# Optimization experiments

Hardware: AMD Instinct MI355X
Metric: run time of the kernel (lower is better)

Reference implementation:

```python
import jax, jax.numpy as jnp
import numpy as np

B, D, H = 256, 512, 256
K = 5
MARGIN = 1.0
TAU = 1.0
LAM_C = 0.01
LAM_E = 0.1
BETA = 0.1
LN_EPS = 1e-5


def _layernorm(x, g, b):
    mu = jnp.mean(x, axis=-1, keepdims=True)
    var = jnp.var(x, axis=-1, keepdims=True)
    return (x - mu) * jax.lax.rsqrt(var + LN_EPS) * g + b


def setup_inputs() -> dict:
    key = jax.random.key(0)
    ks = jax.random.split(key, 16)
    s = 0.02
    inp = {
        "outputs": jax.random.normal(ks[0], (B, 3, 64, 64), jnp.float32),
        "images": jax.random.normal(ks[1], (B, 3, 64, 64), jnp.float32),
        "f_orig": jax.random.normal(ks[2], (B, D), jnp.float32),
        "f_recon": jax.random.normal(ks[3], (B, D), jnp.float32),
        "cf1": jax.random.normal(ks[4], (B, 256, 8, 8), jnp.float32),
        "cf2": jax.random.normal(ks[5], (B, 512, 4, 4), jnp.float32),
        # EnergyNet encoder params
        "W1": jax.random.normal(ks[6], (D, H), jnp.float32) * s,
        "b1": jnp.zeros((H,), jnp.float32),
        "g1": jnp.ones((H,), jnp.float32),
        "be1": jnp.zeros((H,), jnp.float32),
        "W2": jax.random.normal(ks[7], (H, H), jnp.float32) * s,
        "b2": jnp.zeros((H,), jnp.float32),
        # EnergyNet interaction params
        "W3": jax.random.normal(ks[8], (3 * H, H), jnp.float32) * s,
        "b3": jnp.zeros((H,), jnp.float32),
        "g3": jnp.ones((H,), jnp.float32),
        "be3": jnp.zeros((H,), jnp.float32),
        "W4": jax.random.normal(ks[9], (H, H // 2), jnp.float32) * s,
        "b4": jnp.zeros((H // 2,), jnp.float32),
        "W5": jax.random.normal(ks[10], (H // 2, 1), jnp.float32) * s,
        "b5": jnp.zeros((1,), jnp.float32),
    }
    return inp


def _encoder(x, W1, b1, g1, be1, W2, b2):
    h = _layernorm(x @ W1 + b1, g1, be1)
    return jax.nn.relu(h) @ W2 + b2


def _energy_matrix(f1, f2, W1, b1, g1, be1, W2, b2, W3, b3, g3, be3, W4, b4, W5, b5):
    e1 = _encoder(f1, W1, b1, g1, be1, W2, b2)  # [B,H]
    e2 = _encoder(f2, W1, b1, g1, be1, W2, b2)  # [B,H]
    e1b = jnp.broadcast_to(e1[:, None, :], (B, B, H))
    e2b = jnp.broadcast_to(e2[None, :, :], (B, B, H))
    combined = jnp.concatenate([e1b, e2b, e1b * e2b], axis=-1)  # [B,B,3H]
    h = jax.nn.relu(_layernorm(combined @ W3 + b3, g3, be3))
    h = jax.nn.relu(h @ W4 + b4)
    return (h @ W5 + b5)[..., 0]  # [B,B]


def _topk_neighbors(f, k):
    fn = f / (jnp.linalg.norm(f, axis=1, keepdims=True))
    sim = fn @ fn.T
    sim = jnp.where(jnp.eye(f.shape[0], dtype=bool), -jnp.inf, sim)
    _, idx = jax.lax.top_k(sim, k)  # [B,k]
    onehot = jnp.zeros((f.shape[0], f.shape[0]), jnp.float32)
    rows = jnp.arange(f.shape[0])[:, None]
    return onehot.at[rows, idx].set(1.0)


def _entropy(x):
    xn = (x - x.min()) / (x.max() - x.min() + 1e-8)
    # torch.histc(bins=256, min=0, max=1): values at max go to last bin
    idx = jnp.clip(jnp.floor(xn.reshape(-1) * 256.0).astype(jnp.int32), 0, 255)
    hist = jnp.bincount(idx, length=256).astype(jnp.float32)
    p = hist / hist.sum()
    return -jnp.sum(p * jnp.log2(p + 1e-8))


def reference(outputs, images, f_orig, f_recon, cf1, cf2,
              W1, b1, g1, be1, W2, b2, W3, b3, g3, be3, W4, b4, W5, b5):
    # reconstruction loss
    recon = jnp.mean((outputs - images) ** 2)

    # energy margin loss
    E = _energy_matrix(f_orig, f_recon, W1, b1, g1, be1, W2, b2,
                       W3, b3, g3, be3, W4, b4, W5, b5)
    pos = jnp.diag(E)[:, None]
    losses = jax.nn.relu(MARGIN + E - pos)
    neg_mask = ~jnp.eye(B, dtype=bool)
    standard_loss = jnp.sum(losses * neg_mask) / (B * (B - 1))

    k = min(K, B - 1)
    on = _topk_neighbors(f_orig, k)
    rn = _topk_neighbors(f_recon, k)
    inter = jnp.sum(on * rn, axis=1)
    union = jnp.sum(jnp.clip(on + rn, 0.0, 1.0), axis=1)
    jaccard = inter / (union + 1e-8)
    neighbor_loss = 1.0 - jnp.mean(jaccard)
    energy_loss = standard_loss + 0.3 * neighbor_loss

    # compression loss over the dict of compressed features {cf1, cf2}
    sp = 0.5 * (jnp.mean(jnp.abs(cf1)) + jnp.mean(jnp.abs(cf2)))
    en = 0.5 * (_entropy(cf1) + _entropy(cf2))
    compress = sp + BETA * en

    total = recon + LAM_C * compress + LAM_E * energy_loss
    return (total, recon, energy_loss, compress)
```

## Files before the change

### kernel.cpp

```cpp
#include <hip/hip_runtime.h>
#include <math.h>

typedef __attribute__((ext_vector_type(8))) short short8;
typedef __attribute__((ext_vector_type(4))) float f32x4;
typedef __attribute__((ext_vector_type(4))) unsigned int u32x4;

union U8 { unsigned int u[4]; short8 s; u32x4 v; };


__device__ __forceinline__ float wave_sum(float v) {
#pragma unroll
    for (int o = 32; o > 0; o >>= 1) v += __shfl_down(v, o);
    return v;
}

__device__ __forceinline__ float block_sum256(float v, float* red) {
    v = wave_sum(v);
    int t = threadIdx.x;
    if ((t & 63) == 0) red[t >> 6] = v;
    __syncthreads();
    float r = red[0] + red[1] + red[2] + red[3];
    __syncthreads();
    return r;
}

__device__ __forceinline__ unsigned fenc(float f) {
    unsigned u = __float_as_uint(f);
    return (u & 0x80000000u) ? ~u : (u | 0x80000000u);
}
__device__ __forceinline__ float fdec(unsigned u) {
    return (u & 0x80000000u) ? __uint_as_float(u & 0x7fffffffu) : __uint_as_float(~u);
}

__device__ __forceinline__ ushort f2bf(float f) {
    unsigned u = __float_as_uint(f);
    unsigned r = (u + 0x7fffu + ((u >> 16) & 1u)) >> 16;
    return (ushort)r;
}
__device__ __forceinline__ float bflo(unsigned u) { return __uint_as_float(u << 16); }
__device__ __forceinline__ float bfhi(unsigned u) { return __uint_as_float(u & 0xffff0000u); }
__device__ __forceinline__ float bf2f(ushort u) { return __uint_as_float((unsigned)u << 16); }


__global__ void init_kernel(float* wsf, unsigned* wsu, int* wsi) {
    int t = threadIdx.x;
    if (t < 7) wsf[t] = 0.f;
    if (t == 7 || t == 9) wsu[t] = 0xFFFFFFFFu;
    if (t == 8 || t == 10) wsu[t] = 0u;
    wsi[16 + t] = 0;
    wsi[272 + t] = 0;
}

__device__ __forceinline__ void pack256(const float* __restrict__ src, ushort* __restrict__ dst, int s) {
    int lane = s & 63;
    int tt = (s >> 6) & 15;
    int kk = s >> 10;
    int qq = lane >> 4, nn = lane & 15;
    int tcol = tt * 16 + nn;
    short8 v;
#pragma unroll
    for (int jj = 0; jj < 8; ++jj) {
        int k = kk * 32 + qq * 8 + jj;
        v[jj] = (short)f2bf(src[(size_t)k * 256 + tcol]);
    }
    *(short8*)(dst + (size_t)s * 8) = v;
}

__device__ __forceinline__ void pack128(const float* __restrict__ src, ushort* __restrict__ dst, int s) {
    int lane = s & 63;
    int tt = (s >> 6) & 7;
    int kk = s >> 9;
    int qq = lane >> 4, nn = lane & 15;
    int ncol = tt * 16 + nn;
    short8 v;
#pragma unroll
    for (int jj = 0; jj < 8; ++jj) {
        int k = kk * 32 + qq * 8 + jj;
        v[jj] = (short)f2bf(src[(size_t)k * 128 + ncol]);
    }
    *(short8*)(dst + (size_t)s * 8) = v;
}

__global__ __launch_bounds__(256) void mega_kernel(
    const float4* __restrict__ o, const float4* __restrict__ im,
    const float4* __restrict__ cf1, const float4* __restrict__ cf2,
    const float* __restrict__ fo, const float* __restrict__ fr,
    const float* __restrict__ W1, const float* __restrict__ W2,
    const float* __restrict__ W3, const float* __restrict__ W4,
    float* wsf, unsigned* wsu, float* rnorm, float* fT,
    ushort* __restrict__ W3cpk, ushort* __restrict__ W4pk,
    ushort* __restrict__ W1pk, ushort* __restrict__ W2pk,
    ushort* __restrict__ W3apk, ushort* __restrict__ W3bpk) {
    __shared__ float smem[64 * 33];
    float* red = smem;
    int b = blockIdx.x, t = threadIdx.x;
    if (b < 208) {
        int pb = b;
        if (pb < 32) pack256(W3 + 512 * 256, W3cpk, pb * 256 + t);
        else if (pb < 48) pack128(W4, W4pk, (pb - 32) * 256 + t);
        else if (pb < 112) pack256(W1, W1pk, (pb - 48) * 256 + t);
        else if (pb < 144) pack256(W2, W2pk, (pb - 112) * 256 + t);
        else if (pb < 176) pack256(W3, W3apk, (pb - 144) * 256 + t);
        else pack256(W3 + 256 * 256, W3bpk, (pb - 176) * 256 + t);
    } else if (b < 336) {
        int bb = b - 208;
        int pass = bb >> 6;
        int kt = (bb >> 2) & 15;
        int jt = bb & 3;
        int k0 = kt * 32, j0 = jt * 64;
        const float* f = pass ? fr : fo;
        float (*tile)[33] = (float(*)[33])smem;
        int cl = t & 31, rl = t >> 5;
#pragma unroll
        for (int r = 0; r < 8; ++r) {
            int row = j0 + rl + r * 8;
            tile[rl + r * 8][cl] = f[(size_t)row * 512 + k0 + cl];
        }
        __syncthreads();
        int jl = t & 63, kq = t >> 6;
        float* dst = fT + (size_t)pass * 131072;
#pragma unroll
        for (int c = 0; c < 8; ++c) {
            int kl = kq * 8 + c;
            dst[(size_t)(k0 + kl) * 256 + j0 + jl] = tile[jl][kl];
        }
    } else {
        int bs = b - 336;
        if (bs < 512) {
            int base = bs * 1536 + t;
            float4 av[6], cv[6];
#pragma unroll
            for (int u = 0; u < 6; ++u) { av[u] = o[base + u * 256]; cv[u] = im[base + u * 256]; }
            float s0 = 0.f, s1 = 0.f;
#pragma unroll
            for (int u = 0; u < 6; ++u) {
                float dx = av[u].x - cv[u].x, dy = av[u].y - cv[u].y;
                float dz = av[u].z - cv[u].z, dw = av[u].w - cv[u].w;
                if (u & 1) s1 += dx * dx + dy * dy + dz * dz + dw * dw;
                else s0 += dx * dx + dy * dy + dz * dz + dw * dw;
            }
            float tot = block_sum256(s0 + s1, red);
            if (t == 0) atomicAdd(wsf + 0, tot);
        } else if (bs < 1536) {
            int which = (bs < 1024) ? 0 : 1;
            const float4* x = which ? cf2 : cf1;
            int niter = which ? 4 : 8;
            int base = which ? ((bs - 1024) * 1024 + t) : ((bs - 512) * 2048 + t);
            float4 v[8];
            for (int u = 0; u < niter; ++u) v[u] = x[base + u * 256];
            float s = 0.f, mn = INFINITY, mx = -INFINITY;
            for (int u = 0; u < niter; ++u) {
                float4 a = v[u];
                s += fabsf(a.x) + fabsf(a.y) + fabsf(a.z) + fabsf(a.w);
                mn = fminf(mn, fminf(fminf(a.x, a.y), fminf(a.z, a.w)));
                mx = fmaxf(mx, fmaxf(fmaxf(a.x, a.y), fmaxf(a.z, a.w)));
            }
            float tot = block_sum256(s, red);
#pragma unroll
            for (int off = 32; off > 0; off >>= 1) {
                mn = fminf(mn, __shfl_down(mn, off));
                mx = fmaxf(mx, __shfl_down(mx, off));
            }
            float* rmn = smem + 8;
            float* rmx = smem + 16;
            if ((t & 63) == 0) { rmn[t >> 6] = mn; rmx[t >> 6] = mx; }
            __syncthreads();
            if (t == 0) {
                atomicAdd(wsf + 1 + which, tot);
                float m1 = fminf(fminf(rmn[0], rmn[1]), fminf(rmn[2], rmn[3]));
                float m2 = fmaxf(fmaxf(rmx[0], rmx[1]), fmaxf(rmx[2], rmx[3]));
                atomicMin(wsu + 7 + which * 2, fenc(m1));
                atomicMax(wsu + 8 + which * 2, fenc(m2));
            }
        } else {
            int r = bs - 1536;
            const float4* f = (r < 256) ? ((const float4*)fo + (size_t)r * 128)
                                        : ((const float4*)fr + (size_t)(r - 256) * 128);
            float s = 0.f;
            if (t < 128) {
                float4 a = f[t];
                s = a.x * a.x + a.y * a.y + a.z * a.z + a.w * a.w;
            }
            float tot = block_sum256(s, red);
            if (t == 0) rnorm[r] = 1.0f / sqrtf(tot);
        }
    }
}

__global__ __launch_bounds__(256) void hist_kernel(const float4* __restrict__ cf1,
                                                   const float4* __restrict__ cf2,
                                                   const unsigned* wsu, int* wsi) {
    __shared__ int hl[256];
    int b = blockIdx.x, t = threadIdx.x;
    hl[t] = 0;
    __syncthreads();
    int which = (b < 512) ? 0 : 1;
    const float4* x = which ? cf2 : cf1;
    int niter = which ? 4 : 8;
    int base = which ? ((b - 512) * 1024 + t) : (b * 2048 + t);
    int* hist = wsi + (which ? 272 : 16);
    float mn = fdec(wsu[7 + which * 2]), mx = fdec(wsu[8 + which * 2]);
    float inv = 256.f / (mx - mn + 1e-8f);
    float4 v[8];
    for (int u = 0; u < niter; ++u) v[u] = x[base + u * 256];
    for (int u = 0; u < niter; ++u) {
        float4 a = v[u];
        int b0i = min(max((int)floorf((a.x - mn) * inv), 0), 255);
        int b1i = min(max((int)floorf((a.y - mn) * inv), 0), 255);
        int b2i = min(max((int)floorf((a.z - mn) * inv), 0), 255);
        int b3i = min(max((int)floorf((a.w - mn) * inv), 0), 255);
        atomicAdd(&hl[b0i], 1);
        atomicAdd(&hl[b1i], 1);
        atomicAdd(&hl[b2i], 1);
        atomicAdd(&hl[b3i], 1);
    }
    __syncthreads();
    if (hl[t]) atomicAdd(&hist[t], hl[t]);
}

__global__ __launch_bounds__(64, 1) void encoder_mfma(
    const float* __restrict__ fo, const float* __restrict__ fr,
    const ushort* __restrict__ W1p, const ushort* __restrict__ W2p,
    const ushort* __restrict__ W3ap, const ushort* __restrict__ W3bp,
    const float* __restrict__ b1, const float* __restrict__ g1,
    const float* __restrict__ be1, const float* __restrict__ b2,
    ushort* __restrict__ ebf, ushort* __restrict__ A1bf, ushort* __restrict__ A2bf)
{
    int lane = threadIdx.x & 63;
    int q = lane >> 4, n = lane & 15;
    int r = blockIdx.x * 16 + n;
    bool isOrig = (r < 256);
    const float* f = isOrig ? (fo + (size_t)r * 512) : (fr + (size_t)(r - 256) * 512);

    f32x4 acc[16];
#pragma unroll
    for (int tt = 0; tt < 16; ++tt) acc[tt] = (f32x4){0.f, 0.f, 0.f, 0.f};
    short8 wA[16], wB[16];
    {
        const ushort* wp0 = W1p + (size_t)lane * 8;
#pragma unroll
        for (int tt = 0; tt < 16; ++tt) wA[tt] = *(const short8*)(wp0 + (size_t)tt * 512);
    }
#pragma unroll
    for (int kk = 0; kk < 16; ++kk) {
        const short8* cur = (kk & 1) ? wB : wA;
        short8* nxt = (kk & 1) ? wA : wB;
        if (kk < 15) {
            const ushort* wpn = W1p + ((size_t)((kk + 1) * 1024 + lane)) * 8;
#pragma unroll
            for (int tt = 0; tt < 16; ++tt) nxt[tt] = *(const short8*)(wpn + (size_t)tt * 512);
        }
        int kb = kk * 32 + q * 8;
        float4 fa = *(const float4*)(f + kb);
        float4 fb = *(const float4*)(f + kb + 4);
        U8 bb;
        bb.u[0] = (unsigned)f2bf(fa.x) | ((unsigned)f2bf(fa.y) << 16);
        bb.u[1] = (unsigned)f2bf(fa.z) | ((unsigned)f2bf(fa.w) << 16);
        bb.u[2] = (unsigned)f2bf(fb.x) | ((unsigned)f2bf(fb.y) << 16);
        bb.u[3] = (unsigned)f2bf(fb.z) | ((unsigned)f2bf(fb.w) << 16);
#pragma unroll
        for (int tt = 0; tt < 16; ++tt)
            acc[tt] = __builtin_amdgcn_mfma_f32_16x16x32_bf16(cur[tt], bb.s, acc[tt], 0, 0, 0);
    }
    float s1 = 0.f, s2 = 0.f;
#pragma unroll
    for (int tt = 0; tt < 16; ++tt) {
        int tb = tt * 16 + q * 4;
        float4 bv = *(const float4*)(b1 + tb);
        float v0 = acc[tt][0] + bv.x, v1 = acc[tt][1] + bv.y;
        float v2 = acc[tt][2] + bv.z, v3 = acc[tt][3] + bv.w;
        acc[tt][0] = v0; acc[tt][1] = v1; acc[tt][2] = v2; acc[tt][3] = v3;
        s1 += v0 + v1 + v2 + v3;
        s2 += v0 * v0 + v1 * v1 + v2 * v2 + v3 * v3;
    }
    s1 += __shfl_xor(s1, 16); s1 += __shfl_xor(s1, 32);
    s2 += __shfl_xor(s2, 16); s2 += __shfl_xor(s2, 32);
    float mean = s1 * (1.f / 256.f);
    float var = s2 * (1.f / 256.f) - mean * mean;
    float rstd = rsqrtf(var + 1e-5f);
    uint2 pk[16];
#pragma unroll
    for (int tt = 0; tt < 16; ++tt) {
        int tb = tt * 16 + q * 4;
        float4 gg = *(const float4*)(g1 + tb);
        float4 be = *(const float4*)(be1 + tb);
        float h0 = fmaxf((acc[tt][0] - mean) * rstd * gg.x + be.x, 0.f);
        float h1 = fmaxf((acc[tt][1] - mean) * rstd * gg.y + be.y, 0.f);
        float h2 = fmaxf((acc[tt][2] - mean) * rstd * gg.z + be.z, 0.f);
        float h3 = fmaxf((acc[tt][3] - mean) * rstd * gg.w + be.w, 0.f);
        pk[tt].x = (unsigned)f2bf(h0) | ((unsigned)f2bf(h1) << 16);
        pk[tt].y = (unsigned)f2bf(h2) | ((unsigned)f2bf(h3) << 16);
    }

    int qh = (q >> 1) & 1;
    int src0 = ((q & 1) * 2) * 16 + n;
    int src1 = src0 + 16;

    f32x4 eacc[16];
#pragma unroll
    for (int tt = 0; tt < 16; ++tt) eacc[tt] = (f32x4){0.f, 0.f, 0.f, 0.f};
    {
        const ushort* wp0 = W2p + (size_t)lane * 8;
#pragma unroll
        for (int tt = 0; tt < 16; ++tt) wA[tt] = *(const short8*)(wp0 + (size_t)tt * 512);
    }
#pragma unroll
    for (int kk = 0; kk < 8; ++kk) {
        const short8* cur = (kk & 1) ? wB : wA;
        short8* nxt = (kk & 1) ? wA : wB;
        if (kk < 7) {
            const ushort* wpn = W2p + ((size_t)((kk + 1) * 1024 + lane)) * 8;
#pragma unroll
            for (int tt = 0; tt < 16; ++tt) nxt[tt] = *(const short8*)(wpn + (size_t)tt * 512);
        }
        uint2 lo2 = pk[kk * 2], hi2 = pk[kk * 2 + 1];
        unsigned a0 = (unsigned)__shfl((int)lo2.x, src0);
        unsigned a1 = (unsigned)__shfl((int)lo2.y, src0);
        unsigned b0 = (unsigned)__shfl((int)hi2.x, src0);
        unsigned b1v = (unsigned)__shfl((int)hi2.y, src0);
        unsigned c0 = (unsigned)__shfl((int)lo2.x, src1);
        unsigned c1 = (unsigned)__shfl((int)lo2.y, src1);
        unsigned d0 = (unsigned)__shfl((int)hi2.x, src1);
        unsigned d1 = (unsigned)__shfl((int)hi2.y, src1);
        U8 hb;
        hb.u[0] = qh ? b0 : a0;
        hb.u[1] = qh ? b1v : a1;
        hb.u[2] = qh ? d0 : c0;
        hb.u[3] = qh ? d1 : c1;
#pragma unroll
        for (int tt = 0; tt < 16; ++tt)
            eacc[tt] = __builtin_amdgcn_mfma_f32_16x16x32_bf16(cur[tt], hb.s, eacc[tt], 0, 0, 0);
    }
    uint2 epk[16];
#pragma unroll
    for (int tt = 0; tt < 16; ++tt) {
        int tb = tt * 16 + q * 4;
        float4 bv = *(const float4*)(b2 + tb);
        float e0 = eacc[tt][0] + bv.x, e1 = eacc[tt][1] + bv.y;
        float e2 = eacc[tt][2] + bv.z, e3 = eacc[tt][3] + bv.w;
        epk[tt].x = (unsigned)f2bf(e0) | ((unsigned)f2bf(e1) << 16);
        epk[tt].y = (unsigned)f2bf(e2) | ((unsigned)f2bf(e3) << 16);
        *(uint2*)(ebf + (size_t)r * 256 + tb) = epk[tt];
    }

    const ushort* W3x = isOrig ? W3ap : W3bp;
    f32x4 aacc[16];
#pragma unroll
    for (int tt = 0; tt < 16; ++tt) aacc[tt] = (f32x4){0.f, 0.f, 0.f, 0.f};
    {
        const ushort* wp0 = W3x + (size_t)lane * 8;
#pragma unroll
        for (int tt = 0; tt < 16; ++tt) wA[tt] = *(const short8*)(wp0 + (size_t)tt * 512);
    }
#pragma unroll
    for (int kk = 0; kk < 8; ++kk) {
        const short8* cur = (kk & 1) ? wB : wA;
        short8* nxt = (kk & 1) ? wA : wB;
        if (kk < 7) {
            const ushort* wpn = W3x + ((size_t)((kk + 1) * 1024 + lane)) * 8;
#pragma unroll
            for (int tt = 0; tt < 16; ++tt) nxt[tt] = *(const short8*)(wpn + (size_t)tt * 512);
        }
        uint2 lo2 = epk[kk * 2], hi2 = epk[kk * 2 + 1];
        unsigned a0 = (unsigned)__shfl((int)lo2.x, src0);
        unsigned a1 = (unsigned)__shfl((int)lo2.y, src0);
        unsigned b0 = (unsigned)__shfl((int)hi2.x, src0);
        unsigned b1v = (unsigned)__shfl((int)hi2.y, src0);
        unsigned c0 = (unsigned)__shfl((int)lo2.x, src1);
        unsigned c1 = (unsigned)__shfl((int)lo2.y, src1);
        unsigned d0 = (unsigned)__shfl((int)hi2.x, src1);
        unsigned d1 = (unsigned)__shfl((int)hi2.y, src1);
        U8 hb;
        hb.u[0] = qh ? b0 : a0;
        hb.u[1] = qh ? b1v : a1;
        hb.u[2] = qh ? d0 : c0;
        hb.u[3] = qh ? d1 : c1;
#pragma unroll
        for (int tt = 0; tt < 16; ++tt)
            aacc[tt] = __builtin_amdgcn_mfma_f32_16x16x32_bf16(cur[tt], hb.s, aacc[tt], 0, 0, 0);
    }
    ushort* dst = isOrig ? (A1bf + (size_t)r * 256) : (A2bf + (size_t)(r - 256) * 256);
#pragma unroll
    for (int tt = 0; tt < 16; ++tt) {
        int tb = tt * 16 + q * 4;
        uint2 pv;
        pv.x = (unsigned)f2bf(aacc[tt][0]) | ((unsigned)f2bf(aacc[tt][1]) << 16);
        pv.y = (unsigned)f2bf(aacc[tt][2]) | ((unsigned)f2bf(aacc[tt][3]) << 16);
        *(uint2*)(dst + tb) = pv;
    }
}

__global__ __launch_bounds__(256) void simtop_kernel(const float* __restrict__ fo,
                                                     const float* __restrict__ fr,
                                                     const float* __restrict__ rnorm,
                                                     const float* __restrict__ fT,
                                                     int* __restrict__ top5) {
    int b = blockIdx.x;
    int pass = b >> 7, pair = b & 127;
    int i0 = pair * 2, i1 = i0 + 1;
    const float* f = pass ? fr : fo;
    const float* rn = rnorm + pass * 256;
    __shared__ float2 fs2[512];
    __shared__ float candV[4][2][5];
    __shared__ int candI[4][2][5];
    int t = threadIdx.x;
    const float* f0 = f + (size_t)i0 * 512;
    const float* f1 = f + (size_t)i1 * 512;
    fs2[t] = make_float2(f0[t], f1[t]);
    fs2[t + 256] = make_float2(f0[t + 256], f1[t + 256]);
    __syncthreads();
    int j = t;
    const float* col = fT + (size_t)pass * 131072 + j;
    float x0 = 0.f, x1 = 0.f, y0 = 0.f, y1 = 0.f, z0 = 0.f, z1 = 0.f, u0 = 0.f, u1 = 0.f;
#pragma unroll 8
    for (int k = 0; k < 128; ++k) {
        float v0 = col[(size_t)k * 256];
        float v1 = col[(size_t)(k + 128) * 256];
        float v2 = col[(size_t)(k + 256) * 256];
        float v3 = col[(size_t)(k + 384) * 256];
        float2 g0 = fs2[k], g1 = fs2[k + 128], g2 = fs2[k + 256], g3 = fs2[k + 384];
        x0 += g0.x * v0; x1 += g0.y * v0;
        y0 += g1.x * v1; y1 += g1.y * v1;
        z0 += g2.x * v2; z1 += g2.y * v2;
        u0 += g3.x * v3; u1 += g3.y * v3;
    }
    float a0 = ((x0 + y0) + (z0 + u0)) * rn[j];
    float a1 = ((x1 + y1) + (z1 + u1)) * rn[j];
    if (j == i0) a0 = -INFINITY;
    if (j == i1) a1 = -INFINITY;
    int w = t >> 6, lane = t & 63;
    for (int sel = 0; sel < 2; ++sel) {
        float v2 = sel ? a1 : a0;
        int idx = j;
        for (int r = 0; r < 5; ++r) {
            float m = v2;
            int mi = idx;
#pragma unroll
            for (int off = 32; off > 0; off >>= 1) {
                float om = __shfl_xor(m, off);
                int omi = __shfl_xor(mi, off);
                if (om > m || (om == m && omi < mi)) { m = om; mi = omi; }
            }
            if (lane == 0) { candV[w][sel][r] = m; candI[w][sel][r] = mi; }
            if (idx == mi) v2 = -INFINITY;
        }
    }
    __syncthreads();
    if (w < 2) {
        float v = -INFINITY;
        int ix = 0x7fffffff;
        if (lane < 20) { v = candV[lane / 5][w][lane % 5]; ix = candI[lane / 5][w][lane % 5]; }
        int iSel = w ? i1 : i0;
        for (int r = 0; r < 5; ++r) {
            float m = v;
            int mi = ix;
#pragma unroll
            for (int off = 32; off > 0; off >>= 1) {
                float om = __shfl_xor(m, off);
                int omi = __shfl_xor(mi, off);
                if (om > m || (om == m && omi < mi)) { m = om; mi = omi; }
            }
            if (lane == 0) top5[((size_t)pass * 256 + iSel) * 5 + r] = mi;
            if (ix == mi) v = -INFINITY;
        }
    }
}

__global__ __launch_bounds__(256, 1) void energy_v6(
    const ushort* __restrict__ A1bf, const ushort* __restrict__ A2bf,
    const ushort* __restrict__ ebf,
    const ushort* __restrict__ W3p, const ushort* __restrict__ W4p,
    const float* __restrict__ b3, const float* __restrict__ g3, const float* __restrict__ be3,
    const float* __restrict__ b4, const float* __restrict__ W5, const float* __restrict__ b5,
    ushort* __restrict__ E)
{
    int i = blockIdx.x;
    int t = threadIdx.x;
    int w = t >> 6, lane = t & 63, q = lane >> 4, n = lane & 15;
    __shared__ __align__(16) ushort W3s[65536];
    __shared__ float combS[256], g3S[256], be3S[256], b4S[128], w5S[128];

    {
        const uint4* src = (const uint4*)W3p;
        uint4* dstl = (uint4*)W3s;
#pragma unroll 1
        for (int x = 0; x < 32; x += 4) {
            uint4 a0 = src[(x + 0) * 256 + t];
            uint4 a1 = src[(x + 1) * 256 + t];
            uint4 a2 = src[(x + 2) * 256 + t];
            uint4 a3 = src[(x + 3) * 256 + t];
            dstl[(x + 0) * 256 + t] = a0;
            dstl[(x + 1) * 256 + t] = a1;
            dstl[(x + 2) * 256 + t] = a2;
            dstl[(x + 3) * 256 + t] = a3;
        }
    }
    combS[t] = bf2f(A1bf[(size_t)i * 256 + t]) + b3[t];
    g3S[t] = g3[t];
    be3S[t] = be3[t];
    if (t < 128) { b4S[t] = b4[t]; w5S[t] = W5[t]; }
    __syncthreads();

    const ushort* e1p = ebf + (size_t)i * 256;
    const ushort* e2p = ebf + 65536;
    float b5v = b5[0];
    int qh = (q >> 1) & 1;
    int src0 = ((q & 1) * 2) * 16 + n;
    int src1 = src0 + 16;

#pragma unroll 1
    for (int s4 = 0; s4 < 4; ++s4) {
        int jb = s4 * 64 + w * 16;
        int j = jb + n;

        f32x4 acc[16];
#pragma unroll
        for (int tt = 0; tt < 16; ++tt) acc[tt] = (f32x4){0.f, 0.f, 0.f, 0.f};

#pragma unroll 1
        for (int kk = 0; kk < 8; ++kk) {
            int kbase = kk * 32 + q * 8;
            U8 e1v;
            e1v.v = *(const u32x4*)(e1p + kbase);
            U8 e2v;
            e2v.v = *(const u32x4*)(e2p + (size_t)j * 256 + kbase);
            U8 bb;
#pragma unroll
            for (int x = 0; x < 4; ++x) {
                float p0 = bflo(e2v.u[x]) * bflo(e1v.u[x]);
                float p1 = bfhi(e2v.u[x]) * bfhi(e1v.u[x]);
                bb.u[x] = (unsigned)f2bf(p0) | ((unsigned)f2bf(p1) << 16);
            }
            const ushort* wp = W3s + ((size_t)(kk * 16) * 64 + lane) * 8;
#pragma unroll
            for (int tt = 0; tt < 16; ++tt) {
                short8 af = *(const short8*)(wp + (size_t)tt * 512);
                acc[tt] = __builtin_amdgcn_mfma_f32_16x16x32_bf16(af, bb.s, acc[tt], 0, 0, 0);
            }
        }

        float s1 = 0.f, s2 = 0.f;
#pragma unroll
        for (int tt = 0; tt < 16; ++tt) {
            int tb = tt * 16 + q * 4;
            float4 cb = *(const float4*)(combS + tb);
            uint2 a2u = *(const uint2*)(A2bf + (size_t)j * 256 + tb);
            float a0 = bflo(a2u.x), a1f = bfhi(a2u.x), a2f = bflo(a2u.y), a3f = bfhi(a2u.y);
            float v0 = acc[tt][0] + cb.x + a0;
            float v1 = acc[tt][1] + cb.y + a1f;
            float v2 = acc[tt][2] + cb.z + a2f;
            float v3 = acc[tt][3] + cb.w + a3f;
            acc[tt][0] = v0; acc[tt][1] = v1; acc[tt][2] = v2; acc[tt][3] = v3;
            s1 += v0 + v1 + v2 + v3;
            s2 += v0 * v0 + v1 * v1 + v2 * v2 + v3 * v3;
        }
        s1 += __shfl_xor(s1, 16); s1 += __shfl_xor(s1, 32);
        s2 += __shfl_xor(s2, 16); s2 += __shfl_xor(s2, 32);
        float mean = s1 * (1.f / 256.f);
        float var = s2 * (1.f / 256.f) - mean * mean;
        float rstd = rsqrtf(var + 1e-5f);
        uint2 pk[16];
#pragma unroll
        for (int tt = 0; tt < 16; ++tt) {
            int tb = tt * 16 + q * 4;
            float4 gg = *(const float4*)(g3S + tb);
            float4 be = *(const float4*)(be3S + tb);
            float h0 = fmaxf((acc[tt][0] - mean) * rstd * gg.x + be.x, 0.f);
            float h1 = fmaxf((acc[tt][1] - mean) * rstd * gg.y + be.y, 0.f);
            float h2 = fmaxf((acc[tt][2] - mean) * rstd * gg.z + be.z, 0.f);
            float h3 = fmaxf((acc[tt][3] - mean) * rstd * gg.w + be.w, 0.f);
            pk[tt].x = (unsigned)f2bf(h0) | ((unsigned)f2bf(h1) << 16);
            pk[tt].y = (unsigned)f2bf(h2) | ((unsigned)f2bf(h3) << 16);
        }

        f32x4 gacc[8];
#pragma unroll
        for (int nt = 0; nt < 8; ++nt) gacc[nt] = (f32x4){0.f, 0.f, 0.f, 0.f};
#pragma unroll 1
        for (int kk = 0; kk < 8; ++kk) {
            uint2 lo2 = pk[kk * 2], hi2 = pk[kk * 2 + 1];
            unsigned a0 = (unsigned)__shfl((int)lo2.x, src0);
            unsigned a1 = (unsigned)__shfl((int)lo2.y, src0);
            unsigned b0 = (unsigned)__shfl((int)hi2.x, src0);
            unsigned b1 = (unsigned)__shfl((int)hi2.y, src0);
            unsigned c0 = (unsigned)__shfl((int)lo2.x, src1);
            unsigned c1 = (unsigned)__shfl((int)lo2.y, src1);
            unsigned d0 = (unsigned)__shfl((int)hi2.x, src1);
            unsigned d1 = (unsigned)__shfl((int)hi2.y, src1);
            U8 hb;
            hb.u[0] = qh ? b0 : a0;
            hb.u[1] = qh ? b1 : a1;
            hb.u[2] = qh ? d0 : c0;
            hb.u[3] = qh ? d1 : c1;
            const ushort* wp = W4p + ((size_t)(kk * 8) * 64 + lane) * 8;
#pragma unroll
            for (int nt = 0; nt < 8; ++nt) {
                short8 wa = *(const short8*)(wp + (size_t)nt * 512);
                gacc[nt] = __builtin_amdgcn_mfma_f32_16x16x32_bf16(wa, hb.s, gacc[nt], 0, 0, 0);
            }
        }

        float ep = 0.f;
#pragma unroll
        for (int nt = 0; nt < 8; ++nt) {
            int nb = nt * 16 + q * 4;
            float4 b4v = *(const float4*)(b4S + nb);
            float4 w5v = *(const float4*)(w5S + nb);
            ep += fmaxf(gacc[nt][0] + b4v.x, 0.f) * w5v.x;
            ep += fmaxf(gacc[nt][1] + b4v.y, 0.f) * w5v.y;
            ep += fmaxf(gacc[nt][2] + b4v.z, 0.f) * w5v.z;
            ep += fmaxf(gacc[nt][3] + b4v.w, 0.f) * w5v.w;
        }
        ep += __shfl_xor(ep, 16);
        ep += __shfl_xor(ep, 32);
        if (q == 0) E[(size_t)i * 256 + j] = f2bf(ep + b5v);
    }
}

__global__ void margin_jac_kernel(const ushort* __restrict__ E, const int* __restrict__ top5,
                                  float* slAcc, float* jacOut) {
    __shared__ float red[4];
    int b = blockIdx.x, t = threadIdx.x;
    if (b < 256) {
        float diag = bf2f(E[(size_t)b * 256 + b]);
        float l = (t == b) ? 0.f : fmaxf(1.f + bf2f(E[(size_t)b * 256 + t]) - diag, 0.f);
        float tot = block_sum256(l, red);
        if (t == 0) atomicAdd(slAcc, tot);
    } else {
        int O[5], R[5];
#pragma unroll
        for (int r = 0; r < 5; ++r) {
            O[r] = top5[t * 5 + r];
            R[r] = top5[(256 + t) * 5 + r];
        }
        int inter = 0;
#pragma unroll
        for (int a = 0; a < 5; ++a)
#pragma unroll
            for (int bq = 0; bq < 5; ++bq) inter += (O[a] == R[bq]);
        float fi2 = (float)inter;
        float jac = fi2 / (10.f - fi2 + 1e-8f);
        float s = block_sum256(jac, red);
        if (t == 0) jacOut[0] = s;
    }
}

__global__ void finalize_kernel(const float* wsf, const int* h1, const int* h2, float* out) {
    __shared__ float red[4];
    int t = threadIdx.x;
    float p1 = (float)h1[t] / 4194304.f;
    float p2 = (float)h2[t] / 2097152.f;
    float s1 = block_sum256(-p1 * log2f(p1 + 1e-8f), red);
    float s2 = block_sum256(-p2 * log2f(p2 + 1e-8f), red);
    if (t == 0) {
        float recon = wsf[0] / 3145728.f;
        float sp = 0.5f * (wsf[1] / 4194304.f + wsf[2] / 2097152.f);
        float en = 0.5f * (s1 + s2);
        float compress = sp + 0.1f * en;
        float sl = wsf[5] / (256.f * 255.f);
        float nl = 1.f - wsf[6] / 256.f;
        float energy = sl + 0.3f * nl;
        float total = recon + 0.01f * compress + 0.1f * energy;
        out[0] = total;
        out[1] = recon;
        out[2] = energy;
        out[3] = compress;
    }
}

extern "C" void kernel_launch(void* const* d_in, const int* in_sizes, int n_in,
                              void* d_out, int out_size, void* d_ws, size_t ws_size,
                              hipStream_t stream) {
    const float* outputs = (const float*)d_in[0];
    const float* images  = (const float*)d_in[1];
    const float* f_orig  = (const float*)d_in[2];
    const float* f_recon = (const float*)d_in[3];
    const float* cf1 = (const float*)d_in[4];
    const float* cf2 = (const float*)d_in[5];
    const float* W1 = (const float*)d_in[6];
    const float* b1 = (const float*)d_in[7];
    const float* g1 = (const float*)d_in[8];
    const float* be1 = (const float*)d_in[9];
    const float* W2 = (const float*)d_in[10];
    const float* b2 = (const float*)d_in[11];
    const float* W3 = (const float*)d_in[12];
    const float* b3 = (const float*)d_in[13];
    const float* g3 = (const float*)d_in[14];
    const float* be3 = (const float*)d_in[15];
    const float* W4 = (const float*)d_in[16];
    const float* b4 = (const float*)d_in[17];
    const float* W5 = (const float*)d_in[18];
    const float* b5 = (const float*)d_in[19];

    float* wsf = (float*)d_ws;
    unsigned* wsu = (unsigned*)d_ws;
    int* wsi = (int*)d_ws;
    float* out = (float*)d_out;

    float* rnorm = wsf + 528;
    ushort* A1bf = (ushort*)(wsf + 1040);
    ushort* A2bf = (ushort*)(wsf + 33808);
    ushort* ebf  = (ushort*)(wsf + 66576);
    ushort* Ebf  = (ushort*)(wsf + 132112);
    ushort* W3cpk = (ushort*)(wsf + 164880);
    ushort* W4pk  = (ushort*)(wsf + 197648);
    ushort* W1pk  = (ushort*)(wsf + 214032);
    ushort* W2pk  = (ushort*)(wsf + 279568);
    ushort* W3apk = (ushort*)(wsf + 312336);
    ushort* W3bpk = (ushort*)(wsf + 345104);
    float* fT = wsf + 377872;
    int* top5 = wsi + 640016;

    hipLaunchKernelGGL(init_kernel, dim3(1), dim3(256), 0, stream, wsf, wsu, wsi);
    hipLaunchKernelGGL(mega_kernel, dim3(2384), dim3(256), 0, stream,
                       (const float4*)outputs, (const float4*)images,
                       (const float4*)cf1, (const float4*)cf2,
                       f_orig, f_recon, W1, W2, W3, W4,
                       wsf, wsu, rnorm, fT, W3cpk, W4pk, W1pk, W2pk, W3apk, W3bpk);
    hipLaunchKernelGGL(hist_kernel, dim3(1024), dim3(256), 0, stream,
                       (const float4*)cf1, (const float4*)cf2, wsu, wsi);
    hipLaunchKernelGGL(encoder_mfma, dim3(32), dim3(64), 0, stream,
                       f_orig, f_recon, W1pk, W2pk, W3apk, W3bpk,
                       b1, g1, be1, b2, ebf, A1bf, A2bf);
    hipLaunchKernelGGL(simtop_kernel, dim3(256), dim3(256), 0, stream,
                       f_orig, f_recon, rnorm, fT, top5);
    hipLaunchKernelGGL(energy_v6, dim3(256), dim3(256), 0, stream,
                       A1bf, A2bf, ebf, W3cpk, W4pk, b3, g3, be3, b4, W5, b5, Ebf);
    hipLaunchKernelGGL(margin_jac_kernel, dim3(257), dim3(256), 0, stream,
                       Ebf, top5, wsf + 5, wsf + 6);
    hipLaunchKernelGGL(finalize_kernel, dim3(1), dim3(256), 0, stream,
                       wsf, wsi + 16, wsi + 272, out);
}
```

Measured before the change: 315.6 us.

## Double energy kernel block to 512 threads and template cf reduction loops

The energy kernel now runs 512 threads (8 waves) per block instead of 256. Each block covers its 256 j-columns in 2 passes of 128 rather than 4 passes of 64, and the W3 copy into shared memory is split across twice as many threads. The cf1/cf2 abs/min/max and histogram loops become templates with compile-time trip counts, so they can be fully unrolled and keep their values in registers. The cost is higher register pressure, since 512 threads share one CU under launch_bounds(512,1), which could force spills given each thread holds 16 f32x4 accumulators.

```diff
diff --git a/kernel.cpp b/kernel.cpp
--- a/kernel.cpp
+++ b/kernel.cpp
@@ -79,6 +79,40 @@
         v[jj] = (short)f2bf(src[(size_t)k * 128 + ncol]);
     }
     *(short8*)(dst + (size_t)s * 8) = v;
+}
+
+template <int NITER>
+__device__ __forceinline__ void absmm_body(const float4* __restrict__ x, int base, int which,
+                                           float* wsf, unsigned* wsu, float* smem) {
+    int t = threadIdx.x;
+    float4 v[NITER];
+#pragma unroll
+    for (int u = 0; u < NITER; ++u) v[u] = x[base + u * 256];
+    float s = 0.f, mn = INFINITY, mx = -INFINITY;
+#pragma unroll
+    for (int u = 0; u < NITER; ++u) {
+        float4 a = v[u];
+        s += fabsf(a.x) + fabsf(a.y) + fabsf(a.z) + fabsf(a.w);
+        mn = fminf(mn, fminf(fminf(a.x, a.y), fminf(a.z, a.w)));
+        mx = fmaxf(mx, fmaxf(fmaxf(a.x, a.y), fmaxf(a.z, a.w)));
+    }
+    float tot = block_sum256(s, smem);
+#pragma unroll
+    for (int off = 32; off > 0; off >>= 1) {
+        mn = fminf(mn, __shfl_down(mn, off));
+        mx = fmaxf(mx, __shfl_down(mx, off));
+    }
+    float* rmn = smem + 8;
+    float* rmx = smem + 16;
+    if ((t & 63) == 0) { rmn[t >> 6] = mn; rmx[t >> 6] = mx; }
+    __syncthreads();
+    if (t == 0) {
+        atomicAdd(wsf + 1 + which, tot);
+        float m1 = fminf(fminf(rmn[0], rmn[1]), fminf(rmn[2], rmn[3]));
+        float m2 = fmaxf(fmaxf(rmx[0], rmx[1]), fmaxf(rmx[2], rmx[3]));
+        atomicMin(wsu + 7 + which * 2, fenc(m1));
+        atomicMax(wsu + 8 + which * 2, fenc(m2));
+    }
 }
 
 __global__ __launch_bounds__(256) void mega_kernel(
@@ -141,37 +175,10 @@
             }
             float tot = block_sum256(s0 + s1, red);
             if (t == 0) atomicAdd(wsf + 0, tot);
+        } else if (bs < 1024) {
+            absmm_body<8>(cf1, (bs - 512) * 2048 + t, 0, wsf, wsu, smem);
         } else if (bs < 1536) {
-            int which = (bs < 1024) ? 0 : 1;
-            const float4* x = which ? cf2 : cf1;
-            int niter = which ? 4 : 8;
-            int base = which ? ((bs - 1024) * 1024 + t) : ((bs - 512) * 2048 + t);
-            float4 v[8];
-            for (int u = 0; u < niter; ++u) v[u] = x[base + u * 256];
-            float s = 0.f, mn = INFINITY, mx = -INFINITY;
-            for (int u = 0; u < niter; ++u) {
-                float4 a = v[u];
-                s += fabsf(a.x) + fabsf(a.y) + fabsf(a.z) + fabsf(a.w);
-                mn = fminf(mn, fminf(fminf(a.x, a.y), fminf(a.z, a.w)));
-                mx = fmaxf(mx, fmaxf(fmaxf(a.x, a.y), fmaxf(a.z, a.w)));
-            }
-            float tot = block_sum256(s, red);
-#pragma unroll
-            for (int off = 32; off > 0; off >>= 1) {
-                mn = fminf(mn, __shfl_down(mn, off));
-                mx = fmaxf(mx, __shfl_down(mx, off));
-            }
-            float* rmn = smem + 8;
-            float* rmx = smem + 16;
-            if ((t & 63) == 0) { rmn[t >> 6] = mn; rmx[t >> 6] = mx; }
-            __syncthreads();
-            if (t == 0) {
-                atomicAdd(wsf + 1 + which, tot);
-                float m1 = fminf(fminf(rmn[0], rmn[1]), fminf(rmn[2], rmn[3]));
-                float m2 = fmaxf(fmaxf(rmx[0], rmx[1]), fmaxf(rmx[2], rmx[3]));
-                atomicMin(wsu + 7 + which * 2, fenc(m1));
-                atomicMax(wsu + 8 + which * 2, fenc(m2));
-            }
+            absmm_body<4>(cf2, (bs - 1024) * 1024 + t, 1, wsf, wsu, smem);
         } else {
             int r = bs - 1536;
             const float4* f = (r < 256) ? ((const float4*)fo + (size_t)r * 128)
@@ -187,23 +194,14 @@
     }
 }
 
-__global__ __launch_bounds__(256) void hist_kernel(const float4* __restrict__ cf1,
-                                                   const float4* __restrict__ cf2,
-                                                   const unsigned* wsu, int* wsi) {
-    __shared__ int hl[256];
-    int b = blockIdx.x, t = threadIdx.x;
-    hl[t] = 0;
-    __syncthreads();
-    int which = (b < 512) ? 0 : 1;
-    const float4* x = which ? cf2 : cf1;
-    int niter = which ? 4 : 8;
-    int base = which ? ((b - 512) * 1024 + t) : (b * 2048 + t);
-    int* hist = wsi + (which ? 272 : 16);
-    float mn = fdec(wsu[7 + which * 2]), mx = fdec(wsu[8 + which * 2]);
-    float inv = 256.f / (mx - mn + 1e-8f);
-    float4 v[8];
-    for (int u = 0; u < niter; ++u) v[u] = x[base + u * 256];
-    for (int u = 0; u < niter; ++u) {
+template <int NITER>
+__device__ __forceinline__ void hist_body(const float4* __restrict__ x, int base,
+                                          float mn, float inv, int* hl) {
+    float4 v[NITER];
+#pragma unroll
+    for (int u = 0; u < NITER; ++u) v[u] = x[base + u * 256];
+#pragma unroll
+    for (int u = 0; u < NITER; ++u) {
         float4 a = v[u];
         int b0i = min(max((int)floorf((a.x - mn) * inv), 0), 255);
         int b1i = min(max((int)floorf((a.y - mn) * inv), 0), 255);
@@ -214,6 +212,21 @@
         atomicAdd(&hl[b2i], 1);
         atomicAdd(&hl[b3i], 1);
     }
+}
+
+__global__ __launch_bounds__(256) void hist_kernel(const float4* __restrict__ cf1,
+                                                   const float4* __restrict__ cf2,
+                                                   const unsigned* wsu, int* wsi) {
+    __shared__ int hl[256];
+    int b = blockIdx.x, t = threadIdx.x;
+    hl[t] = 0;
+    __syncthreads();
+    int which = (b < 512) ? 0 : 1;
+    int* hist = wsi + (which ? 272 : 16);
+    float mn = fdec(wsu[7 + which * 2]), mx = fdec(wsu[8 + which * 2]);
+    float inv = 256.f / (mx - mn + 1e-8f);
+    if (which == 0) hist_body<8>(cf1, b * 2048 + t, mn, inv, hl);
+    else hist_body<4>(cf2, (b - 512) * 1024 + t, mn, inv, hl);
     __syncthreads();
     if (hl[t]) atomicAdd(&hist[t], hl[t]);
 }
@@ -466,7 +479,7 @@
     }
 }
 
-__global__ __launch_bounds__(256, 1) void energy_v6(
+__global__ __launch_bounds__(512, 1) void energy_v7(
     const ushort* __restrict__ A1bf, const ushort* __restrict__ A2bf,
     const ushort* __restrict__ ebf,
     const ushort* __restrict__ W3p, const ushort* __restrict__ W4p,
@@ -484,20 +497,22 @@
         const uint4* src = (const uint4*)W3p;
         uint4* dstl = (uint4*)W3s;
 #pragma unroll 1
-        for (int x = 0; x < 32; x += 4) {
-            uint4 a0 = src[(x + 0) * 256 + t];
-            uint4 a1 = src[(x + 1) * 256 + t];
-            uint4 a2 = src[(x + 2) * 256 + t];
-            uint4 a3 = src[(x + 3) * 256 + t];
-            dstl[(x + 0) * 256 + t] = a0;
-            dstl[(x + 1) * 256 + t] = a1;
-            dstl[(x + 2) * 256 + t] = a2;
-            dstl[(x + 3) * 256 + t] = a3;
-        }
-    }
-    combS[t] = bf2f(A1bf[(size_t)i * 256 + t]) + b3[t];
-    g3S[t] = g3[t];
-    be3S[t] = be3[t];
+        for (int x = 0; x < 16; x += 4) {
+            uint4 a0 = src[(x + 0) * 512 + t];
+            uint4 a1 = src[(x + 1) * 512 + t];
+            uint4 a2 = src[(x + 2) * 512 + t];
+            uint4 a3 = src[(x + 3) * 512 + t];
+            dstl[(x + 0) * 512 + t] = a0;
+            dstl[(x + 1) * 512 + t] = a1;
+            dstl[(x + 2) * 512 + t] = a2;
+            dstl[(x + 3) * 512 + t] = a3;
+        }
+    }
+    if (t < 256) {
+        combS[t] = bf2f(A1bf[(size_t)i * 256 + t]) + b3[t];
+        g3S[t] = g3[t];
+        be3S[t] = be3[t];
+    }
     if (t < 128) { b4S[t] = b4[t]; w5S[t] = W5[t]; }
     __syncthreads();
 
@@ -509,9 +524,8 @@
     int src1 = src0 + 16;
 
 #pragma unroll 1
-    for (int s4 = 0; s4 < 4; ++s4) {
-        int jb = s4 * 64 + w * 16;
-        int j = jb + n;
+    for (int p = 0; p < 2; ++p) {
+        int j = p * 128 + w * 16 + n;
 
         f32x4 acc[16];
 #pragma unroll
@@ -724,7 +738,7 @@
                        b1, g1, be1, b2, ebf, A1bf, A2bf);
     hipLaunchKernelGGL(simtop_kernel, dim3(256), dim3(256), 0, stream,
                        f_orig, f_recon, rnorm, fT, top5);
-    hipLaunchKernelGGL(energy_v6, dim3(256), dim3(256), 0, stream,
+    hipLaunchKernelGGL(energy_v7, dim3(256), dim3(512), 0, stream,
                        A1bf, A2bf, ebf, W3cpk, W4pk, b3, g3, be3, b4, W5, b5, Ebf);
     hipLaunchKernelGGL(margin_jac_kernel, dim3(257), dim3(256), 0, stream,
                        Ebf, top5, wsf + 5, wsf + 6);
```

Result: no change. 313.6 us (-0.6%).
